# Kernel tuning notes

Measured on AMD Instinct MI355X. Metric: run time of the kernel, lower is better.

The kernel has to match this reference:

```python
import jax, jax.numpy as jnp
import numpy as np

N_NODES = 100000
N_EDGES = 1600000
D_IN = 64
D_OUT = 64
ROW_WINDOW = 16  # TCGNN row-window size (metadata only)


def setup_inputs() -> dict:
    key = jax.random.key(0)
    ks = jax.random.split(key, 7)
    X = jax.random.normal(ks[0], (N_NODES, D_IN), dtype=jnp.float32)
    weights = jax.random.normal(ks[1], (D_IN, D_OUT), dtype=jnp.float32)
    # CSR row pointers: sorted offsets into the edge list, endpoints pinned.
    rp = jnp.sort(jax.random.randint(ks[2], (N_NODES + 1,), 0, N_EDGES, dtype=jnp.int32))
    row_pointers = rp.at[0].set(0).at[-1].set(N_EDGES)
    column_index = jax.random.randint(ks[3], (N_EDGES,), 0, N_NODES, dtype=jnp.int32)
    # TCGNN tiling metadata (does not affect the math; kept for signature fidelity)
    blockPartition = jax.random.randint(ks[4], (N_NODES // ROW_WINDOW,), 0, 8, dtype=jnp.int32)
    edgeToColumn = jax.random.randint(ks[5], (N_EDGES,), 0, N_NODES, dtype=jnp.int32)
    edgeToRow = jax.random.randint(ks[6], (N_EDGES,), 0, N_NODES, dtype=jnp.int32)
    return {
        "X": X,
        "weights": weights,
        "row_pointers": row_pointers,
        "column_index": column_index,
        "blockPartition": blockPartition,
        "edgeToColumn": edgeToColumn,
        "edgeToRow": edgeToRow,
    }


def reference(X, weights, row_pointers, column_index, blockPartition, edgeToColumn, edgeToRow):
    # TCGNN.forward == unweighted CSR SpMM: X_prime[i] = sum_{j in N(i)} X[j]
    n_edges = column_index.shape[0]
    # Map each edge position to its CSR row id.
    row_ids = jnp.searchsorted(row_pointers, jnp.arange(n_edges, dtype=row_pointers.dtype), side="right") - 1
    gathered = X[column_index]  # [n_edges, d_in] irregular gather
    X_prime = jax.ops.segment_sum(gathered, row_ids, num_segments=X.shape[0])  # [n_nodes, d_in]
    return X_prime @ weights  # dense GEMM [n_nodes, d_out]
```

## Files before the change

### kernel.cpp

```cpp
#include <hip/hip_runtime.h>
#include <cstdint>
#include <cstddef>

#define D 64

typedef float    f32x4 __attribute__((ext_vector_type(4)));
typedef short    s16x8 __attribute__((ext_vector_type(8)));
typedef uint32_t u32x4 __attribute__((ext_vector_type(4)));

__device__ __forceinline__ uint32_t rne_bf16(float f) {
    uint32_t x = __float_as_uint(f);
    return (x + 0x7fffu + ((x >> 16) & 1u)) >> 16;
}
__device__ __forceinline__ float bf16lo(uint32_t u) { return __uint_as_float(u << 16); }
__device__ __forceinline__ float bf16hi(uint32_t u) { return __uint_as_float(u & 0xffff0000u); }

__global__ __launch_bounds__(256) void cast_kernel(
    const float* __restrict__ X, uint32_t* __restrict__ Xh, long n4)
{
    long i = (long)blockIdx.x * blockDim.x + threadIdx.x;
    const long stride = (long)gridDim.x * blockDim.x;
    for (; i < n4; i += stride) {
        f32x4 v = __builtin_nontemporal_load((const f32x4*)X + i);
        uint2 o;
        o.x = rne_bf16(v.x) | (rne_bf16(v.y) << 16);
        o.y = rne_bf16(v.z) | (rne_bf16(v.w) << 16);
        ((uint2*)Xh)[i] = o;
    }
}

__global__ __launch_bounds__(256) void gather3_kernel(
    const uint32_t* __restrict__ Xh, const int* __restrict__ rp,
    const int* __restrict__ ci, uint32_t* __restrict__ Agg, int n_nodes)
{
    const int lane = threadIdx.x & 63;
    const int o = lane >> 3;
    const int p = lane & 7;
    const int row = (int)((blockIdx.x * blockDim.x + threadIdx.x) >> 6);
    if (row >= n_nodes) return;

    const int e0 = rp[row];
    const int e1 = rp[row + 1];

    float a[8] = {0,0,0,0,0,0,0,0};
    float b[8] = {0,0,0,0,0,0,0,0};

    int e = e0;
    for (; e + 32 <= e1; e += 32) {
        const int i0 = ci[e      + o];
        const int i1 = ci[e +  8 + o];
        const int i2 = ci[e + 16 + o];
        const int i3 = ci[e + 24 + o];
        const u32x4 u0 = *(const u32x4*)(Xh + (size_t)i0 * 32 + p * 4);
        const u32x4 u1 = *(const u32x4*)(Xh + (size_t)i1 * 32 + p * 4);
        const u32x4 u2 = *(const u32x4*)(Xh + (size_t)i2 * 32 + p * 4);
        const u32x4 u3 = *(const u32x4*)(Xh + (size_t)i3 * 32 + p * 4);
#pragma unroll
        for (int k = 0; k < 4; ++k) {
            a[2*k] += bf16lo(u0[k]); a[2*k+1] += bf16hi(u0[k]);
            b[2*k] += bf16lo(u1[k]); b[2*k+1] += bf16hi(u1[k]);
            a[2*k] += bf16lo(u2[k]); a[2*k+1] += bf16hi(u2[k]);
            b[2*k] += bf16lo(u3[k]); b[2*k+1] += bf16hi(u3[k]);
        }
    }
    if (e + 16 <= e1) {
        const int i0 = ci[e     + o];
        const int i1 = ci[e + 8 + o];
        const u32x4 u0 = *(const u32x4*)(Xh + (size_t)i0 * 32 + p * 4);
        const u32x4 u1 = *(const u32x4*)(Xh + (size_t)i1 * 32 + p * 4);
#pragma unroll
        for (int k = 0; k < 4; ++k) {
            a[2*k] += bf16lo(u0[k]); a[2*k+1] += bf16hi(u0[k]);
            b[2*k] += bf16lo(u1[k]); b[2*k+1] += bf16hi(u1[k]);
        }
        e += 16;
    }
    if (e + 8 <= e1) {
        const int i0 = ci[e + o];
        const u32x4 u0 = *(const u32x4*)(Xh + (size_t)i0 * 32 + p * 4);
#pragma unroll
        for (int k = 0; k < 4; ++k) {
            a[2*k] += bf16lo(u0[k]); a[2*k+1] += bf16hi(u0[k]);
        }
        e += 8;
    }
    if (o < e1 - e) {
        const int i0 = ci[e + o];
        const u32x4 u0 = *(const u32x4*)(Xh + (size_t)i0 * 32 + p * 4);
#pragma unroll
        for (int k = 0; k < 4; ++k) {
            b[2*k] += bf16lo(u0[k]); b[2*k+1] += bf16hi(u0[k]);
        }
    }

#pragma unroll
    for (int j = 0; j < 8; ++j) {
        float v = a[j] + b[j];
        v += __shfl_xor(v, 8, 64);
        v += __shfl_xor(v, 16, 64);
        v += __shfl_xor(v, 32, 64);
        a[j] = v;
    }
    if (lane < 8) {
        u32x4 w;
#pragma unroll
        for (int k = 0; k < 4; ++k)
            w[k] = rne_bf16(a[2*k]) | (rne_bf16(a[2*k+1]) << 16);
        *(u32x4*)(Agg + (size_t)row * 32 + p * 4) = w;
    }
}

__global__ __launch_bounds__(256) void agg_gemm_kernel(
    const uint32_t* __restrict__ Agg, const float* __restrict__ W,
    float* __restrict__ out, int n_nodes)
{
    const int lane = threadIdx.x & 63;
    const int n = lane & 15;
    const int q = lane >> 4;

    s16x8 Bf[4][2];
#pragma unroll
    for (int c = 0; c < 4; ++c)
#pragma unroll
        for (int kb = 0; kb < 2; ++kb) {
            s16x8 bfr;
#pragma unroll
            for (int j = 0; j < 8; ++j) {
                const int k = kb * 32 + q * 8 + j;
                bfr[j] = (short)rne_bf16(W[k * D + c * 16 + n]);
            }
            Bf[c][kb] = bfr;
        }

    const int n_tiles = (n_nodes + 15) / 16;
    const int gwave = (int)((blockIdx.x * blockDim.x + threadIdx.x) >> 6);
    const int nwaves = (int)((gridDim.x * blockDim.x) >> 6);

    for (int t = gwave; t < n_tiles; t += nwaves) {
        const int m0 = t * 16;
        int arow = m0 + n;
        if (arow >= n_nodes) arow = n_nodes - 1;
        const s16x8 A0 = *(const s16x8*)(Agg + (size_t)arow * 32 + q * 4);
        const s16x8 A1 = *(const s16x8*)(Agg + (size_t)arow * 32 + 16 + q * 4);

        f32x4 acc[4];
#pragma unroll
        for (int c = 0; c < 4; ++c) {
            f32x4 z = {0.f, 0.f, 0.f, 0.f};
            z = __builtin_amdgcn_mfma_f32_16x16x32_bf16(A0, Bf[c][0], z, 0, 0, 0);
            z = __builtin_amdgcn_mfma_f32_16x16x32_bf16(A1, Bf[c][1], z, 0, 0, 0);
            acc[c] = z;
        }
#pragma unroll
        for (int r = 0; r < 4; ++r) {
            const int ro = m0 + q * 4 + r;
            if (ro < n_nodes) {
#pragma unroll
                for (int c = 0; c < 4; ++c)
                    out[(size_t)ro * D + c * 16 + n] = acc[c][r];
            }
        }
    }
}

__global__ __launch_bounds__(256) void fused_kernel(
    const float* __restrict__ X, const float* __restrict__ W,
    const int* __restrict__ rp, const int* __restrict__ ci,
    float* __restrict__ out, int n_nodes)
{
    __shared__ float Wl[D * D];
    for (int i = threadIdx.x; i < D * D; i += 256) Wl[i] = W[i];
    __syncthreads();

    const int lane = threadIdx.x & 63;
    const int gwave = (int)((blockIdx.x * blockDim.x + threadIdx.x) >> 6);
    const int nwaves = (int)((gridDim.x * blockDim.x) >> 6);

    for (int row = gwave; row < n_nodes; row += nwaves) {
        int e0 = rp[row];
        int e1 = rp[row + 1];
        float acc = 0.f;
        for (int e = e0; e < e1; ++e) acc += X[ci[e] * D + lane];
        float sum = 0.f;
#pragma unroll
        for (int d = 0; d < D; ++d) {
            float a = __shfl(acc, d, 64);
            sum += a * Wl[d * D + lane];
        }
        out[row * D + lane] = sum;
    }
}

extern "C" void kernel_launch(void* const* d_in, const int* in_sizes, int n_in,
                              void* d_out, int out_size, void* d_ws, size_t ws_size,
                              hipStream_t stream)
{
    const float* X  = (const float*)d_in[0];
    const float* W  = (const float*)d_in[1];
    const int*   rp = (const int*)d_in[2];
    const int*   ci = (const int*)d_in[3];
    float* out = (float*)d_out;

    const int n_nodes = in_sizes[2] - 1;
    const size_t row_bytes = 32 * sizeof(uint32_t);
    const size_t need = 2 * (size_t)n_nodes * row_bytes;

    if (ws_size >= need) {
        uint32_t* Xh  = (uint32_t*)d_ws;
        uint32_t* Agg = (uint32_t*)((char*)d_ws + (size_t)n_nodes * row_bytes);

        const long n4 = (long)n_nodes * (D / 4);
        int cast_blocks = (int)((n4 + 255) / 256);
        if (cast_blocks > 6400) cast_blocks = 6400;
        cast_kernel<<<cast_blocks, 256, 0, stream>>>(X, Xh, n4);

        const int gather_blocks = (n_nodes + 3) / 4;
        gather3_kernel<<<gather_blocks, 256, 0, stream>>>(Xh, rp, ci, Agg, n_nodes);

        const int n_tiles = (n_nodes + 15) / 16;
        const int gemm_blocks = (n_tiles + 3) / 4;
        agg_gemm_kernel<<<gemm_blocks, 256, 0, stream>>>(Agg, W, out, n_nodes);
    } else {
        fused_kernel<<<2048, 256, 0, stream>>>(X, W, rp, ci, out, n_nodes);
    }
}
```

Before: 146.7 us.

## Reorder to gather(X·W): fuse cast into dense GEMM, gather writes fp32 output

Uses associativity to compute X·W first, folding the bf16 cast of X into an MFMA GEMM that writes a bf16 XW buffer. The sparse gather then sums XW rows and writes the fp32 output directly. This goes from three kernels to two and drops the separate Agg round trip. The risk is that bf16 rounding now happens after the GEMM rather than before it, and the output stores are scattered per row instead of MFMA-tiled.

```diff
diff --git a/kernel.cpp b/kernel.cpp
--- a/kernel.cpp
+++ b/kernel.cpp
@@ -15,23 +15,70 @@
 __device__ __forceinline__ float bf16lo(uint32_t u) { return __uint_as_float(u << 16); }
 __device__ __forceinline__ float bf16hi(uint32_t u) { return __uint_as_float(u & 0xffff0000u); }
 
-__global__ __launch_bounds__(256) void cast_kernel(
-    const float* __restrict__ X, uint32_t* __restrict__ Xh, long n4)
-{
-    long i = (long)blockIdx.x * blockDim.x + threadIdx.x;
-    const long stride = (long)gridDim.x * blockDim.x;
-    for (; i < n4; i += stride) {
-        f32x4 v = __builtin_nontemporal_load((const f32x4*)X + i);
-        uint2 o;
-        o.x = rne_bf16(v.x) | (rne_bf16(v.y) << 16);
-        o.y = rne_bf16(v.z) | (rne_bf16(v.w) << 16);
-        ((uint2*)Xh)[i] = o;
-    }
-}
-
-__global__ __launch_bounds__(256) void gather3_kernel(
-    const uint32_t* __restrict__ Xh, const int* __restrict__ rp,
-    const int* __restrict__ ci, uint32_t* __restrict__ Agg, int n_nodes)
+__global__ __launch_bounds__(256) void xw_gemm_kernel(
+    const float* __restrict__ X, const float* __restrict__ W,
+    uint32_t* __restrict__ XWh, int n_nodes)
+{
+    const int lane = threadIdx.x & 63;
+    const int n = lane & 15;
+    const int q = lane >> 4;
+
+    s16x8 Af[4][2];
+#pragma unroll
+    for (int c = 0; c < 4; ++c)
+#pragma unroll
+        for (int kb = 0; kb < 2; ++kb) {
+            s16x8 af;
+#pragma unroll
+            for (int j = 0; j < 8; ++j) {
+                const int k = kb * 32 + q * 8 + j;
+                af[j] = (short)rne_bf16(W[k * D + c * 16 + n]);
+            }
+            Af[c][kb] = af;
+        }
+
+    const int n_tiles = (n_nodes + 15) / 16;
+    const int gwave = (int)((blockIdx.x * blockDim.x + threadIdx.x) >> 6);
+    const int nwaves = (int)((gridDim.x * blockDim.x) >> 6);
+
+    for (int t = gwave; t < n_tiles; t += nwaves) {
+        const int m0 = t * 16;
+        int arow = m0 + n;
+        if (arow >= n_nodes) arow = n_nodes - 1;
+        const float* xp = X + (size_t)arow * D;
+
+        s16x8 Bf[2];
+#pragma unroll
+        for (int kb = 0; kb < 2; ++kb) {
+            const f32x4 x0 = __builtin_nontemporal_load((const f32x4*)(xp + kb * 32 + q * 8));
+            const f32x4 x1 = __builtin_nontemporal_load((const f32x4*)(xp + kb * 32 + q * 8 + 4));
+            s16x8 b;
+            b[0] = (short)rne_bf16(x0.x); b[1] = (short)rne_bf16(x0.y);
+            b[2] = (short)rne_bf16(x0.z); b[3] = (short)rne_bf16(x0.w);
+            b[4] = (short)rne_bf16(x1.x); b[5] = (short)rne_bf16(x1.y);
+            b[6] = (short)rne_bf16(x1.z); b[7] = (short)rne_bf16(x1.w);
+            Bf[kb] = b;
+        }
+
+        const bool live = (m0 + n) < n_nodes;
+#pragma unroll
+        for (int c = 0; c < 4; ++c) {
+            f32x4 z = {0.f, 0.f, 0.f, 0.f};
+            z = __builtin_amdgcn_mfma_f32_16x16x32_bf16(Af[c][0], Bf[0], z, 0, 0, 0);
+            z = __builtin_amdgcn_mfma_f32_16x16x32_bf16(Af[c][1], Bf[1], z, 0, 0, 0);
+            if (live) {
+                uint2 o;
+                o.x = rne_bf16(z[0]) | (rne_bf16(z[1]) << 16);
+                o.y = rne_bf16(z[2]) | (rne_bf16(z[3]) << 16);
+                *(uint2*)(XWh + (size_t)(m0 + n) * 32 + c * 8 + q * 2) = o;
+            }
+        }
+    }
+}
+
+__global__ __launch_bounds__(256) void gather_out_kernel(
+    const uint32_t* __restrict__ XWh, const int* __restrict__ rp,
+    const int* __restrict__ ci, float* __restrict__ out, int n_nodes)
 {
     const int lane = threadIdx.x & 63;
     const int o = lane >> 3;
@@ -51,10 +98,10 @@
         const int i1 = ci[e +  8 + o];
         const int i2 = ci[e + 16 + o];
         const int i3 = ci[e + 24 + o];
-        const u32x4 u0 = *(const u32x4*)(Xh + (size_t)i0 * 32 + p * 4);
-        const u32x4 u1 = *(const u32x4*)(Xh + (size_t)i1 * 32 + p * 4);
-        const u32x4 u2 = *(const u32x4*)(Xh + (size_t)i2 * 32 + p * 4);
-        const u32x4 u3 = *(const u32x4*)(Xh + (size_t)i3 * 32 + p * 4);
+        const u32x4 u0 = *(const u32x4*)(XWh + (size_t)i0 * 32 + p * 4);
+        const u32x4 u1 = *(const u32x4*)(XWh + (size_t)i1 * 32 + p * 4);
+        const u32x4 u2 = *(const u32x4*)(XWh + (size_t)i2 * 32 + p * 4);
+        const u32x4 u3 = *(const u32x4*)(XWh + (size_t)i3 * 32 + p * 4);
 #pragma unroll
         for (int k = 0; k < 4; ++k) {
             a[2*k] += bf16lo(u0[k]); a[2*k+1] += bf16hi(u0[k]);
@@ -66,8 +113,8 @@
     if (e + 16 <= e1) {
         const int i0 = ci[e     + o];
         const int i1 = ci[e + 8 + o];
-        const u32x4 u0 = *(const u32x4*)(Xh + (size_t)i0 * 32 + p * 4);
-        const u32x4 u1 = *(const u32x4*)(Xh + (size_t)i1 * 32 + p * 4);
+        const u32x4 u0 = *(const u32x4*)(XWh + (size_t)i0 * 32 + p * 4);
+        const u32x4 u1 = *(const u32x4*)(XWh + (size_t)i1 * 32 + p * 4);
 #pragma unroll
         for (int k = 0; k < 4; ++k) {
             a[2*k] += bf16lo(u0[k]); a[2*k+1] += bf16hi(u0[k]);
@@ -77,7 +124,7 @@
     }
     if (e + 8 <= e1) {
         const int i0 = ci[e + o];
-        const u32x4 u0 = *(const u32x4*)(Xh + (size_t)i0 * 32 + p * 4);
+        const u32x4 u0 = *(const u32x4*)(XWh + (size_t)i0 * 32 + p * 4);
 #pragma unroll
         for (int k = 0; k < 4; ++k) {
             a[2*k] += bf16lo(u0[k]); a[2*k+1] += bf16hi(u0[k]);
@@ -86,7 +133,7 @@
     }
     if (o < e1 - e) {
         const int i0 = ci[e + o];
-        const u32x4 u0 = *(const u32x4*)(Xh + (size_t)i0 * 32 + p * 4);
+        const u32x4 u0 = *(const u32x4*)(XWh + (size_t)i0 * 32 + p * 4);
 #pragma unroll
         for (int k = 0; k < 4; ++k) {
             b[2*k] += bf16lo(u0[k]); b[2*k+1] += bf16hi(u0[k]);
@@ -102,64 +149,10 @@
         a[j] = v;
     }
     if (lane < 8) {
-        u32x4 w;
-#pragma unroll
-        for (int k = 0; k < 4; ++k)
-            w[k] = rne_bf16(a[2*k]) | (rne_bf16(a[2*k+1]) << 16);
-        *(u32x4*)(Agg + (size_t)row * 32 + p * 4) = w;
-    }
-}
-
-__global__ __launch_bounds__(256) void agg_gemm_kernel(
-    const uint32_t* __restrict__ Agg, const float* __restrict__ W,
-    float* __restrict__ out, int n_nodes)
-{
-    const int lane = threadIdx.x & 63;
-    const int n = lane & 15;
-    const int q = lane >> 4;
-
-    s16x8 Bf[4][2];
-#pragma unroll
-    for (int c = 0; c < 4; ++c)
-#pragma unroll
-        for (int kb = 0; kb < 2; ++kb) {
-            s16x8 bfr;
-#pragma unroll
-            for (int j = 0; j < 8; ++j) {
-                const int k = kb * 32 + q * 8 + j;
-                bfr[j] = (short)rne_bf16(W[k * D + c * 16 + n]);
-            }
-            Bf[c][kb] = bfr;
-        }
-
-    const int n_tiles = (n_nodes + 15) / 16;
-    const int gwave = (int)((blockIdx.x * blockDim.x + threadIdx.x) >> 6);
-    const int nwaves = (int)((gridDim.x * blockDim.x) >> 6);
-
-    for (int t = gwave; t < n_tiles; t += nwaves) {
-        const int m0 = t * 16;
-        int arow = m0 + n;
-        if (arow >= n_nodes) arow = n_nodes - 1;
-        const s16x8 A0 = *(const s16x8*)(Agg + (size_t)arow * 32 + q * 4);
-        const s16x8 A1 = *(const s16x8*)(Agg + (size_t)arow * 32 + 16 + q * 4);
-
-        f32x4 acc[4];
-#pragma unroll
-        for (int c = 0; c < 4; ++c) {
-            f32x4 z = {0.f, 0.f, 0.f, 0.f};
-            z = __builtin_amdgcn_mfma_f32_16x16x32_bf16(A0, Bf[c][0], z, 0, 0, 0);
-            z = __builtin_amdgcn_mfma_f32_16x16x32_bf16(A1, Bf[c][1], z, 0, 0, 0);
-            acc[c] = z;
-        }
-#pragma unroll
-        for (int r = 0; r < 4; ++r) {
-            const int ro = m0 + q * 4 + r;
-            if (ro < n_nodes) {
-#pragma unroll
-                for (int c = 0; c < 4; ++c)
-                    out[(size_t)ro * D + c * 16 + n] = acc[c][r];
-            }
-        }
+        f32x4 w0 = {a[0], a[1], a[2], a[3]};
+        f32x4 w1 = {a[4], a[5], a[6], a[7]};
+        *(f32x4*)(out + (size_t)row * D + p * 8)     = w0;
+        *(f32x4*)(out + (size_t)row * D + p * 8 + 4) = w1;
     }
 }
 
@@ -203,23 +196,15 @@
 
     const int n_nodes = in_sizes[2] - 1;
     const size_t row_bytes = 32 * sizeof(uint32_t);
-    const size_t need = 2 * (size_t)n_nodes * row_bytes;
+    const size_t need = (size_t)n_nodes * row_bytes;
 
     if (ws_size >= need) {
-        uint32_t* Xh  = (uint32_t*)d_ws;
-        uint32_t* Agg = (uint32_t*)((char*)d_ws + (size_t)n_nodes * row_bytes);
-
-        const long n4 = (long)n_nodes * (D / 4);
-        int cast_blocks = (int)((n4 + 255) / 256);
-        if (cast_blocks > 6400) cast_blocks = 6400;
-        cast_kernel<<<cast_blocks, 256, 0, stream>>>(X, Xh, n4);
+        uint32_t* XWh = (uint32_t*)d_ws;
+
+        xw_gemm_kernel<<<1024, 256, 0, stream>>>(X, W, XWh, n_nodes);
 
         const int gather_blocks = (n_nodes + 3) / 4;
-        gather3_kernel<<<gather_blocks, 256, 0, stream>>>(Xh, rp, ci, Agg, n_nodes);
-
-        const int n_tiles = (n_nodes + 15) / 16;
-        const int gemm_blocks = (n_tiles + 3) / 4;
-        agg_gemm_kernel<<<gemm_blocks, 256, 0, stream>>>(Agg, W, out, n_nodes);
+        gather_out_kernel<<<gather_blocks, 256, 0, stream>>>(XWh, rp, ci, out, n_nodes);
     } else {
         fused_kernel<<<2048, 256, 0, stream>>>(X, W, rp, ci, out, n_nodes);
     }
```

New measurement: 141.0 us (median of 2 runs). -3.9%, faster.
